# Kernel tuning notes

Measured on AMD Instinct MI355X. Metric: run time of the kernel, lower is better.

The kernel has to match this reference:

```python
import jax, jax.numpy as jnp
import numpy as np

TOP_P = 0.9  # forward default arg, fixed to exercise the top-p path


def setup_inputs() -> dict:
    key = jax.random.key(0)
    k1, k2 = jax.random.split(key)
    B, V = 128, 128000
    logits = jax.random.normal(k1, (B, V), dtype=jnp.float32) * 2.0
    # temperatures in [0.5, 1.5) to avoid divide-by-near-zero
    temperatures = jax.random.uniform(k2, (B,), dtype=jnp.float32, minval=0.5, maxval=1.5)
    return {"logits": logits, "temperatures": temperatures, "top_k": 50}


def reference(logits, temperatures, top_k):
    B, V = logits.shape
    neg_inf = jnp.float32(-jnp.inf)

    # temperature scale + softmax
    scaled = logits.astype(jnp.float32) / temperatures[:, None]
    probs = jax.nn.softmax(scaled, axis=-1)  # (B, V)

    brow = jnp.arange(B)[:, None]

    # top-k filter: keep top-k probs, fill rest with -inf (matches torch scatter into full(-inf))
    if top_k > 0:
        k = min(top_k, V)
        vals, idx = jax.lax.top_k(probs, k)  # (B, k)
        probs = jnp.full_like(probs, neg_inf).at[brow, idx].set(vals)

    # top-p (nucleus) filter: sort desc, cumsum, mask tail beyond top_p (always keep first)
    if TOP_P < 1.0:
        order = jnp.argsort(-probs, axis=-1)              # descending order indices (-inf sorts last)
        sorted_probs = jnp.take_along_axis(probs, order, axis=-1)
        cum = jnp.cumsum(sorted_probs, axis=-1)
        remove = cum > TOP_P
        remove = remove.at[:, 0].set(False)
        sorted_probs = jnp.where(remove, neg_inf, sorted_probs)
        probs = probs.at[brow, order].set(sorted_probs)   # scatter back to original positions

    # Gumbel-max-style sampling: argmax(probs / Exp(1) noise), noise clamped to >= 1e-10
    kn = jax.random.fold_in(jax.random.key(0), 1)
    noise = jnp.maximum(jax.random.exponential(kn, probs.shape, dtype=jnp.float32), 1e-10)
    return jnp.argmax(probs / noise, axis=-1)  # (B,) int tokens
```

## Files before the change

kernel.cpp:

```cpp
#include <hip/hip_runtime.h>
#include <stdint.h>
#include <limits.h>

#define THREEFRY_PARTITIONABLE 1

#define NTK   1024
#define NWAVE (NTK/64)
#define NBUCK 4096
#define BPT   (NBUCK/NTK)
#define CAP   2048
#define KMAX  512

#if __has_builtin(__builtin_amdgcn_exp2f)
#define FAST_EXP2(x) __builtin_amdgcn_exp2f(x)
#else
#define FAST_EXP2(x) exp2f(x)
#endif

__device__ __forceinline__ uint32_t rotl32(uint32_t v, int r) {
  return (v << r) | (v >> (32 - r));
}
__device__ __forceinline__ void tfround(uint32_t& x0, uint32_t& x1, int r) {
  x0 += x1; x1 = rotl32(x1, r); x1 ^= x0;
}
__device__ __forceinline__ void threefry2x32(uint32_t k0, uint32_t k1,
                                             uint32_t x0, uint32_t x1,
                                             uint32_t& o0, uint32_t& o1) {
  uint32_t k2 = k0 ^ k1 ^ 0x1BD11BDAu;
  x0 += k0; x1 += k1;
  tfround(x0,x1,13); tfround(x0,x1,15); tfround(x0,x1,26); tfround(x0,x1,6);
  x0 += k1; x1 += k2 + 1u;
  tfround(x0,x1,17); tfround(x0,x1,29); tfround(x0,x1,16); tfround(x0,x1,24);
  x0 += k2; x1 += k0 + 2u;
  tfround(x0,x1,13); tfround(x0,x1,15); tfround(x0,x1,26); tfround(x0,x1,6);
  x0 += k0; x1 += k1 + 3u;
  tfround(x0,x1,17); tfround(x0,x1,29); tfround(x0,x1,16); tfround(x0,x1,24);
  x0 += k1; x1 += k2 + 4u;
  tfround(x0,x1,13); tfround(x0,x1,15); tfround(x0,x1,26); tfround(x0,x1,6);
  x0 += k2; x1 += k0 + 5u;
  o0 = x0; o1 = x1;
}
__device__ __forceinline__ float jax_noise(uint32_t kn0, uint32_t kn1,
                                           unsigned long long i,
                                           unsigned long long total) {
  uint32_t o0, o1, bits;
#if THREEFRY_PARTITIONABLE
  threefry2x32(kn0, kn1, (uint32_t)(i >> 32), (uint32_t)(i & 0xFFFFFFFFull), o0, o1);
  bits = o0 ^ o1;
#else
  unsigned long long H = total >> 1;
  if (i < H) { threefry2x32(kn0, kn1, (uint32_t)i, (uint32_t)(i + H), o0, o1); bits = o0; }
  else       { threefry2x32(kn0, kn1, (uint32_t)(i - H), (uint32_t)i, o0, o1); bits = o1; }
#endif
  float u = __uint_as_float((bits >> 9) | 0x3f800000u) - 1.0f;
  float e = -log1pf(-u);
  return fmaxf(e, 1e-10f);
}
__device__ __forceinline__ uint32_t fkey(float f) {
  uint32_t u = __float_as_uint(f);
  return u ^ ((u >> 31) ? 0xFFFFFFFFu : 0x80000000u);
}
__device__ __forceinline__ float unfkey_floor(uint32_t keyT) {
  if (keyT == 0u) return -INFINITY;
  return __uint_as_float((keyT & 0x80000000u) ? (keyT ^ 0x80000000u) : ~keyT);
}
__device__ __forceinline__ int clamp_k(int k) {
  if (k < 1) k = 1;
  if (k > KMAX) k = KMAX;
  return k;
}

__device__ __forceinline__ void block_kth_bucket(uint32_t* hist, uint32_t* wtot,
                                                 int* beta_sh, int k,
                                                 int tid, int lane, int wave) {
  const int base = tid * BPT;
  uint32_t tsum = 0;
#pragma unroll
  for (int j = 0; j < BPT; j++) tsum += hist[base + j];
  uint32_t incl = tsum;
  for (int off = 1; off < 64; off <<= 1) {
    uint32_t v = __shfl_down(incl, off);
    if (lane + off < 64) incl += v;
  }
  if (lane == 0) wtot[wave] = incl;
  __syncthreads();
  uint32_t above = incl - tsum;
  for (int w = wave + 1; w < NWAVE; w++) above += wtot[w];
  if (above < (uint32_t)k && above + tsum >= (uint32_t)k) {
    uint32_t run = above;
    for (int j = BPT - 1; j >= 0; j--) {
      run += hist[base + j];
      if (run >= (uint32_t)k) { *beta_sh = base + j; break; }
    }
  }
  __syncthreads();
}

__global__ __launch_bounds__(NTK, 1)
void sampler_fused(const float* __restrict__ logits,
                   const float* __restrict__ temps,
                   const int* __restrict__ topk_ptr,
                   int* __restrict__ out,
                   int B, int V) {
  const int b = blockIdx.x;
  const int tid = threadIdx.x, lane = tid & 63, wave = tid >> 6;

  __shared__ uint32_t hist[NBUCK];
  __shared__ float cv[CAP];
  __shared__ int   ci[CAP];
  __shared__ float cp[CAP];
  __shared__ float sv[KMAX];
  __shared__ int   si[KMAX];
  __shared__ float sc[KMAX];
  __shared__ float wm[NWAVE];
  __shared__ double wsum[NWAVE];
  __shared__ uint32_t wtot[NWAVE];
  __shared__ int beta_sh, cnum_sh, L_sh;
  __shared__ float m_sh, D_sh;

  if (tid == 0) { beta_sh = 0; cnum_sh = 0; }
  for (int i = tid; i < NBUCK; i += NTK) hist[i] = 0;
  __syncthreads();

  const float T = temps[b];
  const float cf = (float)(1.4426950408889634 / (double)T);
  const int k = clamp_k(*topk_ptr);
  const float* row = logits + (size_t)b * (size_t)V;
  const int n4 = ((V & 3) == 0) ? (V >> 2) : 0;
  const float4* row4 = (const float4*)row;

  float v0 = -INFINITY, v1 = -INFINITY;
  int   i0 = 0, i1 = 0;
  float a0 = 0.f, a1 = 0.f, a2 = 0.f, a3 = 0.f;

  auto proc = [&](float f, int idx) {
    bool gt0 = f > v0;
    bool gt1 = f > v1;
    float nv1 = gt0 ? v0 : (gt1 ? f : v1);
    int   ni1 = gt0 ? i0 : (gt1 ? idx : i1);
    v1 = nv1; i1 = ni1;
    v0 = gt0 ? f : v0;
    i0 = gt0 ? idx : i0;
  };
  auto proc4 = [&](float4 f, int vb, float& a) {
    proc(f.x, vb); proc(f.y, vb + 1); proc(f.z, vb + 2); proc(f.w, vb + 3);
    a += (FAST_EXP2(f.x * cf) + FAST_EXP2(f.y * cf))
       + (FAST_EXP2(f.z * cf) + FAST_EXP2(f.w * cf));
  };

  int i = tid;
  for (; i + 3 * NTK < n4; i += 4 * NTK) {
    float4 fa = row4[i];
    float4 fb = row4[i + NTK];
    float4 fc = row4[i + 2 * NTK];
    float4 fd = row4[i + 3 * NTK];
    proc4(fa, i * 4, a0);
    proc4(fb, (i + NTK) * 4, a1);
    proc4(fc, (i + 2 * NTK) * 4, a2);
    proc4(fd, (i + 3 * NTK) * 4, a3);
  }
  for (; i < n4; i += NTK) {
    float4 fa = row4[i];
    proc4(fa, i * 4, a0);
  }
  for (int v = n4 * 4 + tid; v < V; v += NTK) {
    float f = row[v];
    proc(f, v);
    a0 += FAST_EXP2(f * cf);
  }

  float bm = v0;
  for (int off = 32; off; off >>= 1)
    bm = fmaxf(bm, __shfl_down(bm, off));
  if (lane == 0) wm[wave] = bm;

  double ds = ((double)a0 + (double)a1) + ((double)a2 + (double)a3);
  for (int off = 32; off; off >>= 1)
    ds += __shfl_down(ds, off);
  if (lane == 0) wsum[wave] = ds;

  if (v0 != -INFINITY) atomicAdd(&hist[fkey(v0) >> 20], 1u);
  if (v1 != -INFINITY) atomicAdd(&hist[fkey(v1) >> 20], 1u);
  __syncthreads();

  if (tid == 0) {
    float mg = wm[0];
#pragma unroll
    for (int w = 1; w < NWAVE; w++) mg = fmaxf(mg, wm[w]);
    double t = 0.0;
    for (int w = 0; w < NWAVE; w++) t += wsum[w];
    const double cd = 1.4426950408889634 / (double)T;
    D_sh = (float)(t * exp2(-(double)mg * cd));
    m_sh = mg / T;
  }

  block_kth_bucket(hist, wtot, &beta_sh, k, tid, lane, wave);

  const float fT = unfkey_floor((uint32_t)beta_sh << 20);
  if (v1 >= fT) {
    for (int i2 = tid; i2 < n4; i2 += NTK) {
      float4 f = row4[i2];
      const int vb = i2 * 4;
      if (f.x >= fT) { int p = atomicAdd(&cnum_sh, 1); if (p < CAP) { cv[p] = f.x; ci[p] = vb; } }
      if (f.y >= fT) { int p = atomicAdd(&cnum_sh, 1); if (p < CAP) { cv[p] = f.y; ci[p] = vb + 1; } }
      if (f.z >= fT) { int p = atomicAdd(&cnum_sh, 1); if (p < CAP) { cv[p] = f.z; ci[p] = vb + 2; } }
      if (f.w >= fT) { int p = atomicAdd(&cnum_sh, 1); if (p < CAP) { cv[p] = f.w; ci[p] = vb + 3; } }
    }
    for (int v = n4 * 4 + tid; v < V; v += NTK) {
      float f = row[v];
      if (f >= fT) { int p = atomicAdd(&cnum_sh, 1); if (p < CAP) { cv[p] = f; ci[p] = v; } }
    }
  } else if (v0 >= fT) {
    int p = atomicAdd(&cnum_sh, 1);
    if (p < CAP) { cv[p] = v0; ci[p] = i0; }
  }
  __syncthreads();

  const int C = min(cnum_sh, CAP);
  const float m = m_sh, D = D_sh;
  for (int t = tid; t < C; t += NTK)
    cp[t] = expf(cv[t] / T - m) / D;
  __syncthreads();

  for (int t = tid; t < C; t += NTK) {
    float pi = cp[t];
    int   ii = ci[t];
    int r = 0;
    for (int j = 0; j < C; j++) {
      float pj = cp[j];
      r += (pj > pi) || (pj == pi && ci[j] < ii);
    }
    if (r < k) { sv[r] = pi; si[r] = ii; }
  }
  __syncthreads();

  const int kk = (k < C) ? k : C;
  if (tid == 0) {
    float cum = 0.f;
    int L = 1;
    for (int j = 0; j < kk; j++) {
      cum += sv[j];
      if (j == 0) continue;
      if (cum <= 0.9f) L = j + 1; else break;
    }
    L_sh = L;
  }
  __syncthreads();

  const int L = L_sh;
  {
    uint32_t kn0, kn1;
    threefry2x32(0u, 0u, 0u, 1u, kn0, kn1);
    unsigned long long total = (unsigned long long)B * (unsigned long long)V;
    for (int j = tid; j < L; j += NTK) {
      unsigned long long flat = (unsigned long long)b * (unsigned long long)V
                              + (unsigned long long)si[j];
      sc[j] = sv[j] / jax_noise(kn0, kn1, flat, total);
    }
  }
  __syncthreads();

  if (tid == 0) {
    float bs = -1.0f;
    int   bi = INT_MAX;
    for (int j = 0; j < L; j++) {
      if (sc[j] > bs || (sc[j] == bs && si[j] < bi)) { bs = sc[j]; bi = si[j]; }
    }
    out[b] = bi;
  }
}

extern "C" void kernel_launch(void* const* d_in, const int* in_sizes, int n_in,
                              void* d_out, int out_size, void* d_ws, size_t ws_size,
                              hipStream_t stream) {
  const float* logits = (const float*)d_in[0];
  const float* temps  = (const float*)d_in[1];
  const int*   topk   = (const int*)d_in[2];
  int* out = (int*)d_out;

  int B = in_sizes[1];
  int V = in_sizes[0] / B;

  sampler_fused<<<dim3(B), dim3(NTK), 0, stream>>>(logits, temps, topk, out, B, V);
}
```

Measured before the change: 115.1 us.

## Track top-3 per thread, unroll streaming loops, parallelize final argmax

```diff
diff --git a/kernel.cpp b/kernel.cpp
--- a/kernel.cpp
+++ b/kernel.cpp
@@ -129,15 +129,18 @@
   const int n4 = ((V & 3) == 0) ? (V >> 2) : 0;
   const float4* row4 = (const float4*)row;
 
-  float v0 = -INFINITY, v1 = -INFINITY;
+  float v0 = -INFINITY, v1 = -INFINITY, v2 = -INFINITY;
   int   i0 = 0, i1 = 0;
   float a0 = 0.f, a1 = 0.f, a2 = 0.f, a3 = 0.f;
 
   auto proc = [&](float f, int idx) {
     bool gt0 = f > v0;
     bool gt1 = f > v1;
+    bool gt2 = f > v2;
+    float nv2 = gt1 ? v1 : (gt2 ? f : v2);
     float nv1 = gt0 ? v0 : (gt1 ? f : v1);
     int   ni1 = gt0 ? i0 : (gt1 ? idx : i1);
+    v2 = nv2;
     v1 = nv1; i1 = ni1;
     v0 = gt0 ? f : v0;
     i0 = gt0 ? idx : i0;
@@ -149,6 +152,24 @@
   };
 
   int i = tid;
+  for (; i + 7 * NTK < n4; i += 8 * NTK) {
+    float4 f0 = row4[i];
+    float4 f1 = row4[i + NTK];
+    float4 f2 = row4[i + 2 * NTK];
+    float4 f3 = row4[i + 3 * NTK];
+    float4 f4 = row4[i + 4 * NTK];
+    float4 f5 = row4[i + 5 * NTK];
+    float4 f6 = row4[i + 6 * NTK];
+    float4 f7 = row4[i + 7 * NTK];
+    proc4(f0, i * 4, a0);
+    proc4(f1, (i + NTK) * 4, a1);
+    proc4(f2, (i + 2 * NTK) * 4, a2);
+    proc4(f3, (i + 3 * NTK) * 4, a3);
+    proc4(f4, (i + 4 * NTK) * 4, a0);
+    proc4(f5, (i + 5 * NTK) * 4, a1);
+    proc4(f6, (i + 6 * NTK) * 4, a2);
+    proc4(f7, (i + 7 * NTK) * 4, a3);
+  }
   for (; i + 3 * NTK < n4; i += 4 * NTK) {
     float4 fa = row4[i];
     float4 fb = row4[i + NTK];
@@ -197,22 +218,38 @@
   block_kth_bucket(hist, wtot, &beta_sh, k, tid, lane, wave);
 
   const float fT = unfkey_floor((uint32_t)beta_sh << 20);
-  if (v1 >= fT) {
-    for (int i2 = tid; i2 < n4; i2 += NTK) {
-      float4 f = row4[i2];
-      const int vb = i2 * 4;
-      if (f.x >= fT) { int p = atomicAdd(&cnum_sh, 1); if (p < CAP) { cv[p] = f.x; ci[p] = vb; } }
-      if (f.y >= fT) { int p = atomicAdd(&cnum_sh, 1); if (p < CAP) { cv[p] = f.y; ci[p] = vb + 1; } }
-      if (f.z >= fT) { int p = atomicAdd(&cnum_sh, 1); if (p < CAP) { cv[p] = f.z; ci[p] = vb + 2; } }
-      if (f.w >= fT) { int p = atomicAdd(&cnum_sh, 1); if (p < CAP) { cv[p] = f.w; ci[p] = vb + 3; } }
+  auto emit1 = [&](float f, int idx) {
+    if (f >= fT) {
+      int p = atomicAdd(&cnum_sh, 1);
+      if (p < CAP) { cv[p] = f; ci[p] = idx; }
+    }
+  };
+  auto emit4 = [&](float4 f, int vb) {
+    emit1(f.x, vb); emit1(f.y, vb + 1); emit1(f.z, vb + 2); emit1(f.w, vb + 3);
+  };
+  if (v2 >= fT) {
+    int i2 = tid;
+    for (; i2 + 3 * NTK < n4; i2 += 4 * NTK) {
+      float4 fa = row4[i2];
+      float4 fb = row4[i2 + NTK];
+      float4 fc = row4[i2 + 2 * NTK];
+      float4 fd = row4[i2 + 3 * NTK];
+      emit4(fa, i2 * 4);
+      emit4(fb, (i2 + NTK) * 4);
+      emit4(fc, (i2 + 2 * NTK) * 4);
+      emit4(fd, (i2 + 3 * NTK) * 4);
+    }
+    for (; i2 < n4; i2 += NTK) {
+      float4 fa = row4[i2];
+      emit4(fa, i2 * 4);
     }
     for (int v = n4 * 4 + tid; v < V; v += NTK) {
       float f = row[v];
-      if (f >= fT) { int p = atomicAdd(&cnum_sh, 1); if (p < CAP) { cv[p] = f; ci[p] = v; } }
-    }
-  } else if (v0 >= fT) {
-    int p = atomicAdd(&cnum_sh, 1);
-    if (p < CAP) { cv[p] = v0; ci[p] = i0; }
+      emit1(f, v);
+    }
+  } else {
+    if (v0 >= fT) { int p = atomicAdd(&cnum_sh, 1); if (p < CAP) { cv[p] = v0; ci[p] = i0; } }
+    if (v1 >= fT) { int p = atomicAdd(&cnum_sh, 1); if (p < CAP) { cv[p] = v1; ci[p] = i1; } }
   }
   __syncthreads();
 
@@ -235,38 +272,55 @@
   __syncthreads();
 
   const int kk = (k < C) ? k : C;
-  if (tid == 0) {
-    float cum = 0.f;
-    int L = 1;
-    for (int j = 0; j < kk; j++) {
-      cum += sv[j];
-      if (j == 0) continue;
-      if (cum <= 0.9f) L = j + 1; else break;
-    }
-    L_sh = L;
-  }
-  __syncthreads();
-
-  const int L = L_sh;
+
   {
     uint32_t kn0, kn1;
     threefry2x32(0u, 0u, 0u, 1u, kn0, kn1);
     unsigned long long total = (unsigned long long)B * (unsigned long long)V;
-    for (int j = tid; j < L; j += NTK) {
+    for (int j = tid; j < kk; j += NTK) {
       unsigned long long flat = (unsigned long long)b * (unsigned long long)V
                               + (unsigned long long)si[j];
       sc[j] = sv[j] / jax_noise(kn0, kn1, flat, total);
     }
   }
-  __syncthreads();
 
   if (tid == 0) {
+    float cum = 0.f;
+    int L = 1;
+    bool stop = false;
+    for (int j0 = 0; j0 < kk && !stop; j0 += 8) {
+      float t0 = sv[j0],     t1 = sv[j0 + 1], t2 = sv[j0 + 2], t3 = sv[j0 + 3];
+      float t4 = sv[j0 + 4], t5 = sv[j0 + 5], t6 = sv[j0 + 6], t7 = sv[j0 + 7];
+      float tt[8] = {t0, t1, t2, t3, t4, t5, t6, t7};
+#pragma unroll
+      for (int q = 0; q < 8; q++) {
+        int j = j0 + q;
+        if (j >= kk) { stop = true; break; }
+        cum += tt[q];
+        if (j == 0) continue;
+        if (cum <= 0.9f) L = j + 1;
+        else { stop = true; break; }
+      }
+    }
+    L_sh = L;
+  }
+  __syncthreads();
+
+  if (wave == 0) {
+    const int L = L_sh;
     float bs = -1.0f;
     int   bi = INT_MAX;
-    for (int j = 0; j < L; j++) {
-      if (sc[j] > bs || (sc[j] == bs && si[j] < bi)) { bs = sc[j]; bi = si[j]; }
-    }
-    out[b] = bi;
+    for (int j = lane; j < L; j += 64) {
+      float s = sc[j];
+      int   ix = si[j];
+      if (s > bs || (s == bs && ix < bi)) { bs = s; bi = ix; }
+    }
+    for (int off = 32; off; off >>= 1) {
+      float os = __shfl_down(bs, off);
+      int   oi = __shfl_down(bi, off);
+      if (os > bs || (os == bs && oi < bi)) { bs = os; bi = oi; }
+    }
+    if (lane == 0) out[b] = bi;
   }
 }
 
```

After: 109.9 us. 1.05x faster.
